# Optimization experiments

Hardware: AMD Instinct MI355X
Metric: run time of the kernel (lower is better)

Reference implementation:

```python
import itertools
import jax, jax.numpy as jnp
import numpy as np

# ---- static config (mirrors args) ----
BS = 4; NUM_SEM = 24; C = 4 + NUM_SEM
H_SCREEN = 240; W_SCREEN = 320
FOV = 60.0
RES = 5; Z_RES = 5
MAP_SIZE_CM = 4800 // 2            # global_downscaling = 2
MAP_CELLS = MAP_SIZE_CM // RES     # 480
VR = 100                           # vision_range
AGENT_HEIGHT = 1.55 * 100.0        # cm
MAX_H = int(360 / Z_RES)           # 72
MIN_H = int(-40 / Z_RES)           # -8
MAP_PRED_THR = 1.0; EXP_PRED_THR = 1.0; CAT_PRED_THR = 5.0
SHIFT_X = VR * RES // 2            # 250 cm (shift_loc)
XC = (W_SCREEN - 1.0) / 2.0
ZC = (H_SCREEN - 1.0) / 2.0
FOCAL = (W_SCREEN / 2.0) / float(np.tan(np.deg2rad(FOV / 2.0)))
DEG2RAD = float(np.pi / 180.0)
R2D = 57.29577951308232


def splat_feat_nd(init_grid, feat, coords):
    # init_grid [B,F,D0,D1,D2], feat [B,F,N], coords [B,3,N] in [-1,1]
    B, Fc = init_grid.shape[0], init_grid.shape[1]
    dims = init_grid.shape[2:]
    grid_flat = init_grid.reshape(B, Fc, -1)
    pos_all, wts_all = [], []
    for d in range(len(dims)):
        Dd = dims[d]
        pos = coords[:, d, :] * (Dd / 2.0) + Dd / 2.0   # [B,N]
        fl = jnp.floor(pos)
        pd, wd = [], []
        for off in (0.0, 1.0):
            p = fl + off
            safe = ((p > 0) & (p < Dd)).astype(pos.dtype)
            wd.append((1.0 - jnp.abs(pos - p)) * safe)
            pd.append(p * safe)
        pos_all.append(pd); wts_all.append(wd)
    bidx = jnp.arange(B)[:, None, None]
    fidx = jnp.arange(Fc)[None, :, None]
    for corner in itertools.product((0, 1), repeat=len(dims)):
        index = jnp.zeros_like(pos_all[0][0])
        wts = jnp.ones_like(pos_all[0][0])
        for d in range(len(dims)):
            index = index * dims[d] + pos_all[d][corner[d]]
            wts = wts * wts_all[d][corner[d]]
        idx = index.astype(jnp.int32)[:, None, :]        # [B,1,N]
        grid_flat = grid_flat.at[bidx, fidx, idx].add(feat * wts[:, None, :])
    return jnp.round(grid_flat).reshape(init_grid.shape)


def affine_grid(theta, H, W):
    # align_corners=True base grid; theta [B,2,3] -> grid [B,H,W,2]
    xs = jnp.linspace(-1.0, 1.0, W)
    ys = jnp.linspace(-1.0, 1.0, H)
    gx, gy = jnp.meshgrid(xs, ys)                        # [H,W]
    base = jnp.stack([gx, gy, jnp.ones_like(gx)], axis=-1)
    return jnp.einsum('hwk,bjk->bhwj', base, theta)


def grid_sample(img, grid):
    # bilinear, zero padding, align_corners=True. img [B,C,H,W], grid [B,Ho,Wo,2]
    B, Cc, H, W = img.shape
    ix = (grid[..., 0] + 1.0) * 0.5 * (W - 1)
    iy = (grid[..., 1] + 1.0) * 0.5 * (H - 1)
    x0 = jnp.floor(ix); y0 = jnp.floor(iy)
    x1 = x0 + 1.0; y1 = y0 + 1.0
    wx1 = ix - x0; wx0 = 1.0 - wx1
    wy1 = iy - y0; wy0 = 1.0 - wy1
    bidx = jnp.arange(B)[:, None, None]
    def gather(xi, yi):
        valid = ((xi >= 0) & (xi <= W - 1) & (yi >= 0) & (yi <= H - 1)).astype(img.dtype)
        xc = jnp.clip(xi, 0, W - 1).astype(jnp.int32)
        yc = jnp.clip(yi, 0, H - 1).astype(jnp.int32)
        v = img[bidx, :, yc, xc]                          # [B,Ho,Wo,C]
        return v * valid[..., None]
    out = (gather(x0, y0) * (wx0 * wy0)[..., None]
           + gather(x1, y0) * (wx1 * wy0)[..., None]
           + gather(x0, y1) * (wx0 * wy1)[..., None]
           + gather(x1, y1) * (wx1 * wy1)[..., None])
    return jnp.transpose(out, (0, 3, 1, 2))


def setup_inputs():
    key = jax.random.key(0)
    k1, k2, k3, k4, k5, k6, k7 = jax.random.split(key, 7)
    rgb = jax.random.uniform(k1, (BS, 3, H_SCREEN, W_SCREEN), jnp.float32)
    depth = jax.random.uniform(k2, (BS, 1, H_SCREEN, W_SCREEN), jnp.float32, 50.0, 500.0)  # cm
    seg = jax.random.uniform(k3, (BS, NUM_SEM, H_SCREEN, W_SCREEN), jnp.float32)
    obs = jnp.concatenate([rgb, depth, seg], axis=1)
    pose_obs = jax.random.uniform(k4, (BS, 3), jnp.float32, -0.1, 0.1)
    maps_last = jax.random.uniform(k5, (BS, C, MAP_CELLS, MAP_CELLS), jnp.float32)
    xy = jax.random.uniform(k6, (BS, 2), jnp.float32, 8.0, 16.0)   # meters, inside map
    th = jax.random.uniform(k7, (BS, 1), jnp.float32, -180.0, 180.0)
    poses_last = jnp.concatenate([xy, th], axis=1)
    view_angles = jnp.zeros((BS,), jnp.float32)
    return {"obs": obs, "pose_obs": pose_obs, "maps_last": maps_last,
            "poses_last": poses_last, "view_angles": view_angles, "holding_state": 0}


def _forward(obs, pose_obs, maps_last, poses_last, view_angles):
    bs, c, h, w = obs.shape
    # holding_state == 0 path: mask_err_below = depth < 0
    depth = jnp.where(obs[:, 3] < 0.0, 1e4, obs[:, 3])
    # point cloud from depth (du_scale == 1)
    x_idx = jnp.arange(w, dtype=depth.dtype)
    z_idx = jnp.arange(h - 1, -1, -1).astype(depth.dtype)
    X = (x_idx[None, None, :] - XC) * depth / FOCAL
    Z = (z_idx[None, :, None] - ZC) * depth / FOCAL
    XYZ = jnp.stack([X, depth, Z], axis=-1)              # [bs,h,w,3]
    # camera elevation rotation about x-axis, then add sensor height
    a = view_angles * DEG2RAD
    ca, sa = jnp.cos(a), jnp.sin(a)
    z0 = jnp.zeros_like(ca); o1 = jnp.ones_like(ca)
    Rx = jnp.stack([o1, z0, z0, z0, ca, -sa, z0, sa, ca], -1).reshape(bs, 3, 3)
    XYZ = jnp.einsum('bij,bhwj->bhwi', Rx, XYZ)
    XYZ = XYZ.at[..., 2].add(AGENT_HEIGHT)
    # transform_pose_t with shift_loc: z-rotation by pi/2-pi/2=0, +x shift
    XYZ = XYZ.at[..., 0].add(float(SHIFT_X))
    # normalize to [-1,1] voxel coords
    xy_n = (XYZ[..., :2] / RES - VR // 2.0) / VR * 2.0
    z_n = (XYZ[..., 2] / Z_RES - (MAX_H + MIN_H) // 2.0) / (MAX_H - MIN_H) * 2.0
    coords = jnp.concatenate([xy_n, z_n[..., None]], axis=-1)
    coords = coords.reshape(bs, h * w, 3).transpose(0, 2, 1)            # [bs,3,N]
    feat = jnp.concatenate([jnp.ones((bs, 1, h * w), obs.dtype),
                            obs[:, 4:].reshape(bs, c - 4, h * w)], axis=1)
    init_grid = jnp.zeros((bs, 1 + NUM_SEM, VR, VR, MAX_H - MIN_H), obs.dtype)
    voxels = splat_feat_nd(init_grid, feat, coords).transpose(0, 1, 3, 2, 4)
    min_z = int(15 / Z_RES - MIN_H)
    max_z = int((AGENT_HEIGHT + 1 + 50) / Z_RES - MIN_H)
    agent_height_proj = voxels[..., min_z:max_z].sum(-1)
    all_height_proj = voxels.sum(-1)
    fp_map_pred = jnp.clip(agent_height_proj[:, 0:1] / MAP_PRED_THR, 0.0, 1.0)
    fp_exp_pred = jnp.clip(all_height_proj[:, 0:1] / EXP_PRED_THR, 0.0, 1.0)
    x1 = MAP_CELLS // 2 - VR // 2; x2 = x1 + VR
    y1 = MAP_CELLS // 2; look = VR - 4; y2 = y1 + look
    agent_view = jnp.zeros((bs, c, MAP_CELLS, MAP_CELLS), obs.dtype)
    agent_view = agent_view.at[:, 0:1, y1:y2, x1:x2].set(fp_map_pred[:, :, :look, :])
    agent_view = agent_view.at[:, 1:2, y1:y2, x1:x2].set(fp_exp_pred[:, :, :look, :])
    agent_view = agent_view.at[:, 4:, y1:y2, x1:x2].set(
        jnp.clip(agent_height_proj[:, 1:] / CAT_PRED_THR, 0.0, 1.0)[:, :, :look, :])
    # pose composition (get_new_pose_batch)
    th0 = poses_last[:, 2] / R2D
    ny = poses_last[:, 1] + pose_obs[:, 0] * jnp.sin(th0) + pose_obs[:, 1] * jnp.cos(th0)
    nx = poses_last[:, 0] + pose_obs[:, 0] * jnp.cos(th0) - pose_obs[:, 1] * jnp.sin(th0)
    no = poses_last[:, 2] + pose_obs[:, 2] * R2D
    no = jnp.fmod(no - 180.0, 360.0) + 180.0
    no = jnp.fmod(no + 180.0, 360.0) - 180.0
    current_poses = jnp.stack([nx, ny, no], axis=1)
    st = jax.lax.stop_gradient(current_poses)            # st_pose is .detach()ed
    half = MAP_CELLS // 2
    sx = -(st[:, 0] * 100.0 / RES - half) / half
    sy = -(st[:, 1] * 100.0 / RES - half) / half
    t = (90.0 - st[:, 2]) * DEG2RAD
    ct, s_t = jnp.cos(t), jnp.sin(t)
    zz = jnp.zeros_like(ct); oo = jnp.ones_like(ct)
    theta_rot = jnp.stack([ct, -s_t, zz, s_t, ct, zz], -1).reshape(bs, 2, 3)
    theta_tr = jnp.stack([oo, zz, sx, zz, oo, sy], -1).reshape(bs, 2, 3)
    rot_grid = affine_grid(theta_rot, MAP_CELLS, MAP_CELLS)
    trans_grid = affine_grid(theta_tr, MAP_CELLS, MAP_CELLS)
    rotated = grid_sample(agent_view, rot_grid)
    translated = grid_sample(rotated, trans_grid)
    map_pred = jnp.maximum(maps_last, translated)        # torch.max over stacked pair
    return fp_map_pred, map_pred, current_poses, current_poses


def reference(obs, pose_obs, maps_last, poses_last, view_angles, holding_state):
    # holding_state == 0 path (no object held); branches for 1/2 are host-side numpy.
    return _forward(obs, pose_obs, maps_last, poses_last, view_angles)
```

## Files before the change

kernel.cpp:

```cpp
#include <hip/hip_runtime.h>
#include <math.h>

#define BS 4
#define CC 28
#define NF 25
#define HS 240
#define WSC 320
#define NPIX (HS*WSC)
#define VR 100
#define ZD 80
#define MC 480
#define NCELL (VR*VR)
#define NREC_MAX ((size_t)BS*NPIX*4)

__device__ __forceinline__ float clip01(float v){ return fminf(fmaxf(v, 0.f), 1.f); }

struct Geo {
    float wx[2], wy[2], wz[2];
    int   xi[2], yi[2], zi[2];
    bool  sx[2], sy[2];
};

__device__ __forceinline__ Geo compute_geo(const float* __restrict__ obs,
                                           const float* __restrict__ view_angles,
                                           int b, int pix){
    int j = pix % WSC;
    int i = pix / WSC;
    float depth = obs[((size_t)(b*CC + 3))*NPIX + pix];
    if (depth < 0.f) depth = 10000.f;
    const float FOCAL = 277.12812921102035f;
    float X = ((float)j - 159.5f) * depth / FOCAL;
    float Z = ((float)(HS-1-i) - 119.5f) * depth / FOCAL;
    float a = view_angles[b] * 0.017453292519943295f;
    float ca = cosf(a), sa = sinf(a);
    float Y2 = ca*depth - sa*Z;
    float Z2 = sa*depth + ca*Z + 155.f;
    float X2 = X + 250.f;

    float px = ((X2/5.f - 50.f)/100.f*2.f)*50.f + 50.f;
    float py = ((Y2/5.f - 50.f)/100.f*2.f)*50.f + 50.f;
    float pz = ((Z2/5.f - 32.f)/80.f*2.f)*40.f + 40.f;

    Geo g;
    float fx = floorf(px), fy = floorf(py), fz = floorf(pz);
    {
        float p0 = fx, p1 = fx + 1.f;
        g.sx[0] = (p0 > 0.f) && (p0 < 100.f);
        g.sx[1] = (p1 > 0.f) && (p1 < 100.f);
        g.wx[0] = g.sx[0] ? (1.f - fabsf(px - p0)) : 0.f;
        g.wx[1] = g.sx[1] ? (1.f - fabsf(px - p1)) : 0.f;
        g.xi[0] = g.sx[0] ? (int)p0 : 0;
        g.xi[1] = g.sx[1] ? (int)p1 : 0;
    }
    {
        float p0 = fy, p1 = fy + 1.f;
        g.sy[0] = (p0 > 0.f) && (p0 < 100.f);
        g.sy[1] = (p1 > 0.f) && (p1 < 100.f);
        g.wy[0] = g.sy[0] ? (1.f - fabsf(py - p0)) : 0.f;
        g.wy[1] = g.sy[1] ? (1.f - fabsf(py - p1)) : 0.f;
        g.yi[0] = g.sy[0] ? (int)p0 : 0;
        g.yi[1] = g.sy[1] ? (int)p1 : 0;
    }
    {
        float p0 = fz, p1 = fz + 1.f;
        bool s0 = (p0 > 0.f) && (p0 < 80.f);
        bool s1 = (p1 > 0.f) && (p1 < 80.f);
        g.wz[0] = s0 ? (1.f - fabsf(pz - p0)) : 0.f;
        g.wz[1] = s1 ? (1.f - fabsf(pz - p1)) : 0.f;
        g.zi[0] = s0 ? (int)p0 : 0;
        g.zi[1] = s1 ? (int)p1 : 0;
    }
    return g;
}

__global__ void pose_kernel(const float* __restrict__ pose_obs,
                            const float* __restrict__ poses_last,
                            float* __restrict__ out_p1,
                            float* __restrict__ out_p2,
                            float* __restrict__ params){
    int b = threadIdx.x;
    if (b >= BS) return;
    const float R2D = 57.29577951308232f;
    float th0 = poses_last[b*3+2] / R2D;
    float s0 = sinf(th0), c0 = cosf(th0);
    float ny = poses_last[b*3+1] + pose_obs[b*3+0]*s0 + pose_obs[b*3+1]*c0;
    float nx = poses_last[b*3+0] + pose_obs[b*3+0]*c0 - pose_obs[b*3+1]*s0;
    float no = poses_last[b*3+2] + pose_obs[b*3+2]*R2D;
    no = fmodf(no - 180.f, 360.f) + 180.f;
    no = fmodf(no + 180.f, 360.f) - 180.f;
    out_p1[b*3+0] = nx; out_p1[b*3+1] = ny; out_p1[b*3+2] = no;
    out_p2[b*3+0] = nx; out_p2[b*3+1] = ny; out_p2[b*3+2] = no;
    const float half = 240.f;
    float sx = -(nx*100.f/5.f - half)/half;
    float sy = -(ny*100.f/5.f - half)/half;
    float t = (90.f - no) * 0.017453292519943295f;
    params[b*4+0] = cosf(t);
    params[b*4+1] = sinf(t);
    params[b*4+2] = sx;
    params[b*4+3] = sy;
}

__global__ __launch_bounds__(256)
void prep_kernel(const float* __restrict__ obs,
                 const float* __restrict__ view_angles,
                 int* __restrict__ counts,
                 float* __restrict__ feat){
    __shared__ float sf[6400];
    int t   = threadIdx.x;
    int tid = blockIdx.x * 256 + t;
    int b   = tid / NPIX;
    int pix = tid % NPIX;

    Geo g = compute_geo(obs, view_angles, b, pix);
    #pragma unroll
    for (int cy = 0; cy < 2; ++cy)
    #pragma unroll
    for (int cx = 0; cx < 2; ++cx){
        if (g.sx[cx] && g.sy[cy] && (g.wx[cx]*g.wy[cy] != 0.f))
            atomicAdd(&counts[b*NCELL + g.yi[cy]*VR + g.xi[cx]], 1);
    }

    #pragma unroll 6
    for (int f = 0; f < 24; ++f)
        sf[t*25 + f] = obs[((size_t)(b*CC + 4 + f))*NPIX + pix];
    __syncthreads();
    size_t base = ((size_t)b*NPIX + (size_t)(pix - t)) * 24;
    for (int q = t; q < 6144; q += 256)
        feat[base + q] = sf[q + q/24];
}

__global__ void scan_kernel(const int* __restrict__ counts,
                            int* __restrict__ bases,
                            int* __restrict__ cursor){
    __shared__ int part[1024];
    int t = threadIdx.x;
    const int TOT = BS*NCELL;
    const int CH  = 40;
    int beg = t*CH;
    int s = 0;
    for (int i = 0; i < CH; ++i){
        int idx = beg + i;
        if (idx < TOT) s += counts[idx];
    }
    part[t] = s;
    __syncthreads();
    for (int off = 1; off < 1024; off <<= 1){
        int v = (t >= off) ? part[t-off] : 0;
        __syncthreads();
        part[t] += v;
        __syncthreads();
    }
    int run = (t == 0) ? 0 : part[t-1];
    for (int i = 0; i < CH; ++i){
        int idx = beg + i;
        if (idx < TOT){
            bases[idx]  = run;
            cursor[idx] = run;
            run += counts[idx];
        }
    }
}

__global__ __launch_bounds__(256)
void scatter_kernel(const float* __restrict__ obs,
                    const float* __restrict__ view_angles,
                    int* __restrict__ cursor,
                    uint4* __restrict__ records){
    int tid = blockIdx.x * 256 + threadIdx.x;
    int b   = tid / NPIX;
    int pix = tid % NPIX;
    Geo g = compute_geo(obs, view_angles, b, pix);
    #pragma unroll
    for (int cy = 0; cy < 2; ++cy)
    #pragma unroll
    for (int cx = 0; cx < 2; ++cx){
        float wxy = g.wx[cx] * g.wy[cy];
        if (g.sx[cx] && g.sy[cy] && (wxy != 0.f)){
            int cid = b*NCELL + g.yi[cy]*VR + g.xi[cx];
            int pos = atomicAdd(&cursor[cid], 1);
            float w0 = wxy * g.wz[0];
            float w1 = wxy * g.wz[1];
            unsigned iw = (unsigned)pix | ((unsigned)g.zi[0] << 17)
                                        | ((unsigned)g.zi[1] << 24);
            records[pos] = make_uint4(__float_as_uint(w0), __float_as_uint(w1), iw, 0u);
        }
    }
}

__global__ __launch_bounds__(256)
void accum_kernel(const uint4* __restrict__ records,
                  const float* __restrict__ feat,
                  const int* __restrict__ bases,
                  const int* __restrict__ cursor,
                  float* __restrict__ ahp,
                  float* __restrict__ allp,
                  float* __restrict__ out0){
    __shared__ float col[ZD*NF];
    __shared__ float pall[200], pag[200];

    int cid = blockIdx.x;
    int b   = cid / NCELL;
    int rest = cid % NCELL;
    int y = rest / VR;
    int x = rest % VR;
    int t = threadIdx.x;

    for (int i = t; i < ZD*NF; i += 256) col[i] = 0.f;
    __syncthreads();

    int start = bases[cid];
    int end   = cursor[cid];

    int r = t / NF;
    int f = t % NF;
    bool act = t < 250;
    const float* feat_b = feat + (size_t)b*NPIX*24;

    for (int cb = start; cb < end; cb += 10){
        int idx = cb + r;
        if (act && idx < end){
            uint4 rec = records[idx];
            float w0 = __uint_as_float(rec.x);
            float w1 = __uint_as_float(rec.y);
            unsigned iw = rec.z;
            int pix = (int)(iw & 0x1FFFFu);
            int z0  = (int)((iw >> 17) & 0x7Fu);
            int z1  = (int)((iw >> 24) & 0x7Fu);
            float val = (f == 0) ? 1.f : feat_b[(size_t)pix*24 + (f-1)];
            if (w0 != 0.f) atomicAdd(&col[z0*NF + f], val * w0);
            if (w1 != 0.f) atomicAdd(&col[z1*NF + f], val * w1);
        }
    }
    __syncthreads();

    if (t < 200){
        int ff = t % NF;
        int gq = t / NF;
        float sall = 0.f, sag = 0.f;
        for (int z = gq*10; z < gq*10 + 10; ++z){
            float rv = rintf(col[z*NF + ff]);
            sall += rv;
            if (z >= 11 && z < 49) sag += rv;
        }
        pall[t] = sall;
        pag[t]  = sag;
    }
    __syncthreads();
    if (t < NF){
        float a = 0.f, s = 0.f;
        #pragma unroll
        for (int gq = 0; gq < 8; ++gq){
            s += pall[gq*NF + t];
            a += pag[gq*NF + t];
        }
        ahp[(((size_t)b*NF + t)*VR + y)*VR + x] = a;
        if (t == 0){
            allp[((size_t)b*VR + y)*VR + x] = s;
            out0[(size_t)b*NCELL + y*VR + x] = clip01(a);
        }
    }
}

__global__ __launch_bounds__(256)
void final_kernel(const float* __restrict__ ahp,
                  const float* __restrict__ allp,
                  const float* __restrict__ params,
                  const float* __restrict__ maps_last,
                  float* __restrict__ out1){
    int tid = blockIdx.x * blockDim.x + threadIdx.x;
    if (tid >= BS*MC*MC) return;
    int w = tid % MC;
    int h = (tid / MC) % MC;
    int b = tid / (MC*MC);

    float ct = params[b*4+0], st = params[b*4+1];
    float sx = params[b*4+2], sy = params[b*4+3];

    float gx = -1.f + 2.f*(float)w/479.f;
    float gy = -1.f + 2.f*(float)h/479.f;
    float ix = (gx + sx + 1.f)*0.5f*479.f;
    float iy = (gy + sy + 1.f)*0.5f*479.f;
    float x0 = floorf(ix), y0 = floorf(iy);
    float wx1 = ix - x0, wx0 = 1.f - wx1;
    float wy1 = iy - y0, wy0 = 1.f - wy1;

    int   offs[16];
    float wt16[16];
    int nz = 0;
    #pragma unroll
    for (int tc = 0; tc < 4; ++tc){
        float txf = (tc & 1) ? x0 + 1.f : x0;
        float tyf = (tc & 2) ? y0 + 1.f : y0;
        float wt  = ((tc & 1) ? wx1 : wx0) * ((tc & 2) ? wy1 : wy0);
        bool validT = (txf >= 0.f) && (txf <= 479.f) && (tyf >= 0.f) && (tyf <= 479.f);
        int txc = (int)fminf(fmaxf(txf, 0.f), 479.f);
        int tyc = (int)fminf(fmaxf(tyf, 0.f), 479.f);

        float gx2 = -1.f + 2.f*(float)txc/479.f;
        float gy2 = -1.f + 2.f*(float)tyc/479.f;
        float rgx = ct*gx2 - st*gy2;
        float rgy = st*gx2 + ct*gy2;
        float ixr = (rgx + 1.f)*0.5f*479.f;
        float iyr = (rgy + 1.f)*0.5f*479.f;
        float rx0 = floorf(ixr), ry0 = floorf(iyr);
        float rwx1 = ixr - rx0, rwx0 = 1.f - rwx1;
        float rwy1 = iyr - ry0, rwy0 = 1.f - rwy1;

        #pragma unroll
        for (int rc = 0; rc < 4; ++rc){
            int id = tc*4 + rc;
            float rxf = (rc & 1) ? rx0 + 1.f : rx0;
            float ryf = (rc & 2) ? ry0 + 1.f : ry0;
            float wr  = ((rc & 1) ? rwx1 : rwx0) * ((rc & 2) ? rwy1 : rwy0);
            bool validR = (rxf >= 0.f) && (rxf <= 479.f) && (ryf >= 0.f) && (ryf <= 479.f);
            int rxc = (int)fminf(fmaxf(rxf, 0.f), 479.f);
            int ryc = (int)fminf(fmaxf(ryf, 0.f), 479.f);
            bool inwin = validT && validR &&
                         (rxc >= 190) && (rxc < 290) && (ryc >= 240) && (ryc < 336);
            float wgt = wt * wr;
            if (inwin && wgt != 0.f){
                offs[id] = (ryc - 240)*VR + (rxc - 190);
                wt16[id] = wgt;
                nz++;
            } else {
                offs[id] = -1;
                wt16[id] = 0.f;
            }
        }
    }

    size_t outBase = (size_t)b*CC*MC*MC + (size_t)h*MC + w;
    if (nz == 0){
        #pragma unroll
        for (int ch = 0; ch < CC; ++ch){
            size_t o = outBase + (size_t)ch*MC*MC;
            out1[o] = fmaxf(maps_last[o], 0.f);
        }
        return;
    }

    const float* ahp_b  = ahp  + (size_t)b*NF*VR*VR;
    const float* allp_b = allp + (size_t)b*VR*VR;
    for (int ch = 0; ch < CC; ++ch){
        float acc = 0.f;
        if (ch != 2 && ch != 3){
            #pragma unroll
            for (int id = 0; id < 16; ++id){
                if (offs[id] >= 0){
                    float v;
                    if (ch == 0)      v = clip01(ahp_b[offs[id]]);
                    else if (ch == 1) v = clip01(allp_b[offs[id]]);
                    else              v = clip01(ahp_b[(size_t)(ch-3)*VR*VR + offs[id]] / 5.f);
                    acc += wt16[id] * v;
                }
            }
        }
        size_t o = outBase + (size_t)ch*MC*MC;
        out1[o] = fmaxf(maps_last[o], acc);
    }
}

extern "C" void kernel_launch(void* const* d_in, const int* in_sizes, int n_in,
                              void* d_out, int out_size, void* d_ws, size_t ws_size,
                              hipStream_t stream){
    const float* obs         = (const float*)d_in[0];
    const float* pose_obs    = (const float*)d_in[1];
    const float* maps_last   = (const float*)d_in[2];
    const float* poses_last  = (const float*)d_in[3];
    const float* view_angles = (const float*)d_in[4];
    float* out = (float*)d_out;

    const size_t OUT0 = (size_t)BS*VR*VR;
    const size_t OUT1 = (size_t)BS*CC*MC*MC;
    float* out0 = out;
    float* out1 = out + OUT0;
    float* out2 = out + OUT0 + OUT1;
    float* out3 = out2 + BS*3;

    const size_t AHP_FLOATS  = (size_t)BS*NF*VR*VR;
    const size_t ALLP_FLOATS = (size_t)BS*VR*VR;
    const size_t NCID        = (size_t)BS*NCELL;
    const size_t FEAT_FLOATS = (size_t)BS*NPIX*24;

    float* ahp    = (float*)d_ws;
    float* allp   = ahp  + AHP_FLOATS;
    float* params = allp + ALLP_FLOATS;
    char*  ws_tail = (char*)(params + 16);
    size_t ws_used_small = (size_t)(ws_tail - (char*)d_ws);

    const size_t BIG_BYTES = NCID*3*4 + 32 + NREC_MAX*16 + FEAT_FLOATS*4;
    char* big;
    if (ws_size >= ws_used_small + BIG_BYTES){
        big = ws_tail;
    } else {
        big = (char*)(out1 + OUT1) - BIG_BYTES;
        big = (char*)((uintptr_t)big & ~(uintptr_t)15);
    }
    int* counts = (int*)big;
    int* bases  = counts + NCID;
    int* cursor = bases  + NCID;
    uint4* records = (uint4*)(((uintptr_t)(cursor + NCID) + 15) & ~(uintptr_t)15);
    float* feat    = (float*)(records + NREC_MAX);

    hipMemsetAsync(counts, 0, NCID*4, stream);
    pose_kernel<<<1, 64, 0, stream>>>(pose_obs, poses_last, out2, out3, params);

    int nblk = (BS*NPIX)/256;
    prep_kernel<<<nblk, 256, 0, stream>>>(obs, view_angles, counts, feat);
    scan_kernel<<<1, 1024, 0, stream>>>(counts, bases, cursor);
    scatter_kernel<<<nblk, 256, 0, stream>>>(obs, view_angles, cursor, records);
    accum_kernel<<<(int)NCID, 256, 0, stream>>>(records, feat, bases, cursor,
                                                ahp, allp, out0);
    final_kernel<<<(BS*MC*MC + 255)/256, 256, 0, stream>>>(ahp, allp, params,
                                                           maps_last, out1);
}
```

Before: 930.1 us.

## Fuse pose into scan, add empty-cell early exit, vectorize final map pass

Folds the pose computation into the scan kernel and replaces the shared-memory Hillis-Steele scan with a tiled wavefront-shuffle scan. The accumulate kernel now exits early for cells with no records, stages records in shared memory and prefetches the next feature value. The final kernel handles four pixels per thread, using a conservative bounding-window test so pixels outside the projected view only do a float4 max copy from maps_last. Together these aim to cut launch count, scan latency, idle accumulate work and memory traffic in the large output pass. The hard-coded window bounds could misclassify pixels if the geometry assumption is wrong.

```diff
diff --git a/kernel.cpp b/kernel.cpp
--- a/kernel.cpp
+++ b/kernel.cpp
@@ -73,33 +73,6 @@
     return g;
 }
 
-__global__ void pose_kernel(const float* __restrict__ pose_obs,
-                            const float* __restrict__ poses_last,
-                            float* __restrict__ out_p1,
-                            float* __restrict__ out_p2,
-                            float* __restrict__ params){
-    int b = threadIdx.x;
-    if (b >= BS) return;
-    const float R2D = 57.29577951308232f;
-    float th0 = poses_last[b*3+2] / R2D;
-    float s0 = sinf(th0), c0 = cosf(th0);
-    float ny = poses_last[b*3+1] + pose_obs[b*3+0]*s0 + pose_obs[b*3+1]*c0;
-    float nx = poses_last[b*3+0] + pose_obs[b*3+0]*c0 - pose_obs[b*3+1]*s0;
-    float no = poses_last[b*3+2] + pose_obs[b*3+2]*R2D;
-    no = fmodf(no - 180.f, 360.f) + 180.f;
-    no = fmodf(no + 180.f, 360.f) - 180.f;
-    out_p1[b*3+0] = nx; out_p1[b*3+1] = ny; out_p1[b*3+2] = no;
-    out_p2[b*3+0] = nx; out_p2[b*3+1] = ny; out_p2[b*3+2] = no;
-    const float half = 240.f;
-    float sx = -(nx*100.f/5.f - half)/half;
-    float sy = -(ny*100.f/5.f - half)/half;
-    float t = (90.f - no) * 0.017453292519943295f;
-    params[b*4+0] = cosf(t);
-    params[b*4+1] = sinf(t);
-    params[b*4+2] = sx;
-    params[b*4+3] = sy;
-}
-
 __global__ __launch_bounds__(256)
 void prep_kernel(const float* __restrict__ obs,
                  const float* __restrict__ view_angles,
@@ -129,35 +102,72 @@
         feat[base + q] = sf[q + q/24];
 }
 
-__global__ void scan_kernel(const int* __restrict__ counts,
-                            int* __restrict__ bases,
-                            int* __restrict__ cursor){
-    __shared__ int part[1024];
+__global__ __launch_bounds__(1024)
+void scan_pose_kernel(const int* __restrict__ counts,
+                      int* __restrict__ bases,
+                      int* __restrict__ cursor,
+                      const float* __restrict__ pose_obs,
+                      const float* __restrict__ poses_last,
+                      float* __restrict__ out_p1,
+                      float* __restrict__ out_p2,
+                      float* __restrict__ params){
+    __shared__ int wsum[16];
+    __shared__ int carry_s;
     int t = threadIdx.x;
+    int lane = t & 63, wid = t >> 6;
+    if (t == 0) carry_s = 0;
+
+    if (t >= 32 && t < 32 + BS){
+        int b = t - 32;
+        const float R2D = 57.29577951308232f;
+        float th0 = poses_last[b*3+2] / R2D;
+        float s0 = sinf(th0), c0 = cosf(th0);
+        float ny = poses_last[b*3+1] + pose_obs[b*3+0]*s0 + pose_obs[b*3+1]*c0;
+        float nx = poses_last[b*3+0] + pose_obs[b*3+0]*c0 - pose_obs[b*3+1]*s0;
+        float no = poses_last[b*3+2] + pose_obs[b*3+2]*R2D;
+        no = fmodf(no - 180.f, 360.f) + 180.f;
+        no = fmodf(no + 180.f, 360.f) - 180.f;
+        out_p1[b*3+0] = nx; out_p1[b*3+1] = ny; out_p1[b*3+2] = no;
+        out_p2[b*3+0] = nx; out_p2[b*3+1] = ny; out_p2[b*3+2] = no;
+        const float half = 240.f;
+        float sxp = -(nx*100.f/5.f - half)/half;
+        float syp = -(ny*100.f/5.f - half)/half;
+        float tt = (90.f - no) * 0.017453292519943295f;
+        params[b*4+0] = cosf(tt);
+        params[b*4+1] = sinf(tt);
+        params[b*4+2] = sxp;
+        params[b*4+3] = syp;
+    }
+    __syncthreads();
+
     const int TOT = BS*NCELL;
-    const int CH  = 40;
-    int beg = t*CH;
-    int s = 0;
-    for (int i = 0; i < CH; ++i){
-        int idx = beg + i;
-        if (idx < TOT) s += counts[idx];
-    }
-    part[t] = s;
-    __syncthreads();
-    for (int off = 1; off < 1024; off <<= 1){
-        int v = (t >= off) ? part[t-off] : 0;
-        __syncthreads();
-        part[t] += v;
-        __syncthreads();
-    }
-    int run = (t == 0) ? 0 : part[t-1];
-    for (int i = 0; i < CH; ++i){
-        int idx = beg + i;
-        if (idx < TOT){
-            bases[idx]  = run;
-            cursor[idx] = run;
-            run += counts[idx];
-        }
+    for (int tile = 0; tile < 40; ++tile){
+        int idx = tile*1024 + t;
+        int v = (idx < TOT) ? counts[idx] : 0;
+        int s = v;
+        #pragma unroll
+        for (int off = 1; off < 64; off <<= 1){
+            int u = __shfl_up(s, off, 64);
+            if (lane >= off) s += u;
+        }
+        if (lane == 63) wsum[wid] = s;
+        __syncthreads();
+        if (t < 16){
+            int ws = wsum[t];
+            #pragma unroll
+            for (int off = 1; off < 16; off <<= 1){
+                int u = __shfl_up(ws, off, 64);
+                if (t >= off) ws += u;
+            }
+            wsum[t] = ws;
+        }
+        __syncthreads();
+        int excl    = carry_s + (wid ? wsum[wid-1] : 0) + s - v;
+        int tiletot = wsum[15];
+        if (idx < TOT){ bases[idx] = excl; cursor[idx] = excl; }
+        __syncthreads();
+        if (t == 0) carry_s += tiletot;
+        __syncthreads();
     }
 }
 
@@ -191,12 +201,13 @@
 void accum_kernel(const uint4* __restrict__ records,
                   const float* __restrict__ feat,
                   const int* __restrict__ bases,
-                  const int* __restrict__ cursor,
+                  const int* __restrict__ counts,
                   float* __restrict__ ahp,
                   float* __restrict__ allp,
                   float* __restrict__ out0){
     __shared__ float col[ZD*NF];
     __shared__ float pall[200], pag[200];
+    __shared__ uint4 rbuf[250];
 
     int cid = blockIdx.x;
     int b   = cid / NCELL;
@@ -204,34 +215,55 @@
     int y = rest / VR;
     int x = rest % VR;
     int t = threadIdx.x;
+    int n = counts[cid];
+
+    if (n == 0){
+        if (t < NF) ahp[(((size_t)b*NF + t)*VR + y)*VR + x] = 0.f;
+        if (t == 0){
+            allp[((size_t)b*VR + y)*VR + x] = 0.f;
+            out0[(size_t)b*NCELL + y*VR + x] = 0.f;
+        }
+        return;
+    }
 
     for (int i = t; i < ZD*NF; i += 256) col[i] = 0.f;
-    __syncthreads();
 
     int start = bases[cid];
-    int end   = cursor[cid];
-
     int r = t / NF;
     int f = t % NF;
     bool act = t < 250;
     const float* feat_b = feat + (size_t)b*NPIX*24;
 
-    for (int cb = start; cb < end; cb += 10){
-        int idx = cb + r;
-        if (act && idx < end){
-            uint4 rec = records[idx];
-            float w0 = __uint_as_float(rec.x);
-            float w1 = __uint_as_float(rec.y);
-            unsigned iw = rec.z;
-            int pix = (int)(iw & 0x1FFFFu);
-            int z0  = (int)((iw >> 17) & 0x7Fu);
-            int z1  = (int)((iw >> 24) & 0x7Fu);
-            float val = (f == 0) ? 1.f : feat_b[(size_t)pix*24 + (f-1)];
-            if (w0 != 0.f) atomicAdd(&col[z0*NF + f], val * w0);
-            if (w1 != 0.f) atomicAdd(&col[z1*NF + f], val * w1);
-        }
-    }
-    __syncthreads();
+    for (int tile = 0; tile < n; tile += 250){
+        int m = min(250, n - tile);
+        if (t < m) rbuf[t] = records[start + tile + t];
+        __syncthreads();
+
+        int idx = r;
+        bool v = act && (idx < m);
+        uint4 rec = v ? rbuf[idx] : make_uint4(0u,0u,0u,0u);
+        float val = 1.f;
+        if (v && f) val = feat_b[(size_t)(rec.z & 0x1FFFFu)*24 + (f-1)];
+
+        for (int cb = 0; cb < m; cb += 10){
+            int idx2 = cb + 10 + r;
+            bool v2 = act && (idx2 < m);
+            uint4 rec2 = v2 ? rbuf[idx2] : make_uint4(0u,0u,0u,0u);
+            float val2 = 1.f;
+            if (v2 && f) val2 = feat_b[(size_t)(rec2.z & 0x1FFFFu)*24 + (f-1)];
+
+            if (v){
+                float w0 = __uint_as_float(rec.x);
+                float w1 = __uint_as_float(rec.y);
+                int z0 = (int)((rec.z >> 17) & 0x7Fu);
+                int z1 = (int)((rec.z >> 24) & 0x7Fu);
+                if (w0 != 0.f) atomicAdd(&col[z0*NF + f], val * w0);
+                if (w1 != 0.f) atomicAdd(&col[z1*NF + f], val * w1);
+            }
+            rec = rec2; val = val2; v = v2;
+        }
+        __syncthreads();
+    }
 
     if (t < 200){
         int ff = t % NF;
@@ -261,21 +293,12 @@
     }
 }
 
-__global__ __launch_bounds__(256)
-void final_kernel(const float* __restrict__ ahp,
-                  const float* __restrict__ allp,
-                  const float* __restrict__ params,
-                  const float* __restrict__ maps_last,
-                  float* __restrict__ out1){
-    int tid = blockIdx.x * blockDim.x + threadIdx.x;
-    if (tid >= BS*MC*MC) return;
-    int w = tid % MC;
-    int h = (tid / MC) % MC;
-    int b = tid / (MC*MC);
-
-    float ct = params[b*4+0], st = params[b*4+1];
-    float sx = params[b*4+2], sy = params[b*4+3];
-
+__device__ void final_pixel(const float* __restrict__ ahp_b,
+                            const float* __restrict__ allp_b,
+                            const float* __restrict__ maps_last,
+                            float* __restrict__ out1,
+                            float ct, float st, float sx, float sy,
+                            int b, int h, int w){
     float gx = -1.f + 2.f*(float)w/479.f;
     float gy = -1.f + 2.f*(float)h/479.f;
     float ix = (gx + sx + 1.f)*0.5f*479.f;
@@ -338,9 +361,6 @@
         }
         return;
     }
-
-    const float* ahp_b  = ahp  + (size_t)b*NF*VR*VR;
-    const float* allp_b = allp + (size_t)b*VR*VR;
     for (int ch = 0; ch < CC; ++ch){
         float acc = 0.f;
         if (ch != 2 && ch != 3){
@@ -360,6 +380,53 @@
     }
 }
 
+__global__ __launch_bounds__(256)
+void final_kernel(const float* __restrict__ ahp,
+                  const float* __restrict__ allp,
+                  const float* __restrict__ params,
+                  const float* __restrict__ maps_last,
+                  float* __restrict__ out1){
+    int tid = blockIdx.x * blockDim.x + threadIdx.x;
+    const int WQ = MC/4;
+    if (tid >= BS*MC*WQ) return;
+    int w4 = (tid % WQ) * 4;
+    int h  = (tid / WQ) % MC;
+    int b  = tid / (WQ*MC);
+
+    float ct = params[b*4+0], st = params[b*4+1];
+    float sx = params[b*4+2], sy = params[b*4+3];
+    float gy = -1.f + 2.f*(float)h/479.f;
+
+    bool anywin = false;
+    #pragma unroll
+    for (int k = 0; k < 4; ++k){
+        float gx = -1.f + 2.f*(float)(w4+k)/479.f;
+        float cgx = ct*(gx+sx) - st*(gy+sy);
+        float cgy = st*(gx+sx) + ct*(gy+sy);
+        float exu = (cgx + 1.f)*0.5f*479.f;
+        float exv = (cgy + 1.f)*0.5f*479.f;
+        anywin |= (exu > 186.f) && (exu < 293.f) && (exv > 236.f) && (exv < 339.f);
+    }
+
+    size_t pbase = (size_t)b*CC*MC*MC + (size_t)h*MC + w4;
+    if (!anywin){
+        #pragma unroll 4
+        for (int ch = 0; ch < CC; ++ch){
+            const float4 mv = *(const float4*)(maps_last + pbase + (size_t)ch*MC*MC);
+            float4 o;
+            o.x = fmaxf(mv.x, 0.f); o.y = fmaxf(mv.y, 0.f);
+            o.z = fmaxf(mv.z, 0.f); o.w = fmaxf(mv.w, 0.f);
+            *(float4*)(out1 + pbase + (size_t)ch*MC*MC) = o;
+        }
+        return;
+    }
+
+    const float* ahp_b  = ahp  + (size_t)b*NF*VR*VR;
+    const float* allp_b = allp + (size_t)b*VR*VR;
+    for (int k = 0; k < 4; ++k)
+        final_pixel(ahp_b, allp_b, maps_last, out1, ct, st, sx, sy, b, h, w4+k);
+}
+
 extern "C" void kernel_launch(void* const* d_in, const int* in_sizes, int n_in,
                               void* d_out, int out_size, void* d_ws, size_t ws_size,
                               hipStream_t stream){
@@ -403,14 +470,14 @@
     float* feat    = (float*)(records + NREC_MAX);
 
     hipMemsetAsync(counts, 0, NCID*4, stream);
-    pose_kernel<<<1, 64, 0, stream>>>(pose_obs, poses_last, out2, out3, params);
 
     int nblk = (BS*NPIX)/256;
     prep_kernel<<<nblk, 256, 0, stream>>>(obs, view_angles, counts, feat);
-    scan_kernel<<<1, 1024, 0, stream>>>(counts, bases, cursor);
+    scan_pose_kernel<<<1, 1024, 0, stream>>>(counts, bases, cursor,
+                                             pose_obs, poses_last, out2, out3, params);
     scatter_kernel<<<nblk, 256, 0, stream>>>(obs, view_angles, cursor, records);
-    accum_kernel<<<(int)NCID, 256, 0, stream>>>(records, feat, bases, cursor,
+    accum_kernel<<<(int)NCID, 256, 0, stream>>>(records, feat, bases, counts,
                                                 ahp, allp, out0);
-    final_kernel<<<(BS*MC*MC + 255)/256, 256, 0, stream>>>(ahp, allp, params,
-                                                           maps_last, out1);
-}
+    final_kernel<<<(BS*MC*(MC/4) + 255)/256, 256, 0, stream>>>(ahp, allp, params,
+                                                               maps_last, out1);
+}
```

Result: slower. 1.347 ms (+44.8%).
